# Optimization experiments

Measured on AMD Instinct MI355X. Metric: run time of the kernel, lower is better.

## Reference

```python
import jax, jax.numpy as jnp
import numpy as np

NEG = -9.0e15
EPS = 1e-5  # torch BatchNorm1d default eps


def _chain_idx(n):
    # chain graph with self loops; row-major nonzero ordering (matches torch .nonzero())
    rows, cols = [], []
    for i in range(n):
        for j in (i - 1, i, i + 1):
            if 0 <= j < n:
                rows.append(i); cols.append(j)
    return np.asarray(rows, np.int32), np.asarray(cols, np.int32)


def semgconv(x, W, e, rows, cols, n, b):
    # x: [B,N,Fin]; W: [2,Fin,Fout]; e: [nnz]; returns [B,N,Fout]
    h0 = jnp.einsum('bnf,fo->bno', x, W[0])
    h1 = jnp.einsum('bnf,fo->bno', x, W[1])
    logits = jnp.full((n, n), NEG, x.dtype).at[rows, cols].set(e)
    A = jax.nn.softmax(logits, axis=1)              # row-wise softmax over masked adjacency
    d = jnp.diagonal(A)                             # adj * I contribution
    A_off = A - jnp.diag(d)                         # adj * (1 - I)
    out = d[None, :, None] * h0 + jnp.einsum('ij,bjf->bif', A_off, h1)
    return out + b


def gblock(x, W, e, rows, cols, n, b, g, be):
    # SemGraphConv -> BatchNorm1d (training-mode batch stats over (B,N)) -> ReLU
    h = semgconv(x, W, e, rows, cols, n, b)
    mu = h.mean(axis=(0, 1))
    var = h.var(axis=(0, 1))
    h = g * (h - mu) * jax.lax.rsqrt(var + EPS) + be
    return jax.nn.relu(h)


def setup_inputs() -> dict:
    key = jax.random.key(0)
    ks = iter(jax.random.split(key, 40))
    B, NC, NS, H, HS = 4096, 32, 10, 160, 512  # HS = int(160/10*32)
    rc, cc = _chain_idx(NC)
    rs, cs = _chain_idx(NS)
    nnz_c, nnz_s = len(rc), len(rs)

    def w(shape, scale=0.1):
        return jax.random.normal(next(ks), shape, jnp.float32) * scale

    return dict(
        x_c=jax.random.normal(next(ks), (B, NC, 2), jnp.float32),
        x_s=jax.random.normal(next(ks), (B, NS, 2), jnp.float32),
        W_in=w((2, 2, H)), e_in=w((nnz_c,)) + 1.0, b_in=w((H,)),
        g_in=jnp.ones((H,), jnp.float32), be_in=jnp.zeros((H,), jnp.float32),
        W_s1=w((2, 2, HS)), e_s1=w((nnz_s,)) + 1.0, b_s1=w((HS,)),
        g_s1=jnp.ones((HS,), jnp.float32), be_s1=jnp.zeros((HS,), jnp.float32),
        W_c320=w((3, 2, 2 * H, H)), e_c320=w((3, nnz_c)) + 1.0, b_c320=w((3, H)),
        g_c320=jnp.ones((3, H), jnp.float32), be_c320=jnp.zeros((3, H), jnp.float32),
        W_c160=w((6, 2, H, H)), e_c160=w((6, nnz_c)) + 1.0, b_c160=w((6, H)),
        g_c160=jnp.ones((6, H), jnp.float32), be_c160=jnp.zeros((6, H), jnp.float32),
        W_s512=w((2, 2, HS, HS)), e_s512=w((2, nnz_s)) + 1.0, b_s512=w((2, HS)),
        g_s512=jnp.ones((2, HS), jnp.float32), be_s512=jnp.zeros((2, HS), jnp.float32),
        W_out=w((2, H, 2)), e_out=w((nnz_c,)) + 1.0, b_out=w((2,)),
        mc_r=jnp.asarray(rc), mc_c=jnp.asarray(cc),
        ms_r=jnp.asarray(rs), ms_c=jnp.asarray(cs),
    )


def reference(x_c, x_s, W_in, e_in, b_in, g_in, be_in,
              W_s1, e_s1, b_s1, g_s1, be_s1,
              W_c320, e_c320, b_c320, g_c320, be_c320,
              W_c160, e_c160, b_c160, g_c160, be_c160,
              W_s512, e_s512, b_s512, g_s512, be_s512,
              W_out, e_out, b_out, mc_r, mc_c, ms_r, ms_c):
    B, NC, NS, H = x_c.shape[0], 32, 10, 160
    c = gblock(x_c, W_in, e_in, mc_r, mc_c, NC, b_in, g_in, be_in)
    s = gblock(x_s, W_s1, e_s1, ms_r, ms_c, NS, b_s1, g_s1, be_s1)   # [B,10,512]
    for i in range(3):  # c_block1..3 interleaved with s_block2..3
        s_r = jnp.transpose(s, (0, 2, 1)).reshape(B, NC, H)          # [B,512,10] -> [B,32,160]
        c = gblock(jnp.concatenate([c, s_r], axis=2),
                   W_c320[i], e_c320[i], mc_r, mc_c, NC,
                   b_c320[i], g_c320[i], be_c320[i])
        h = gblock(c, W_c160[2 * i], e_c160[2 * i], mc_r, mc_c, NC,
                   b_c160[2 * i], g_c160[2 * i], be_c160[2 * i])
        h = gblock(h, W_c160[2 * i + 1], e_c160[2 * i + 1], mc_r, mc_c, NC,
                   b_c160[2 * i + 1], g_c160[2 * i + 1], be_c160[2 * i + 1])
        c = c + h                                                     # _ResGraphConv residual
        if i < 2:
            s = gblock(s, W_s512[i], e_s512[i], ms_r, ms_c, NS,
                       b_s512[i], g_s512[i], be_s512[i])
    return jax.nn.sigmoid(semgconv(c, W_out, e_out, mc_r, mc_c, NC, b_out))
```

## Files before the change

### kernel.cpp

```cpp
#include <hip/hip_runtime.h>
#include <hip/hip_bf16.h>

typedef __hip_bfloat16 bf16;
typedef unsigned short u16;
typedef __attribute__((ext_vector_type(8))) short short8;
typedef __attribute__((ext_vector_type(8))) unsigned short u16x8;
typedef __attribute__((ext_vector_type(4))) float f32x4;

#define B_SZ  4096
#define NCN   32
#define NSN   10
#define MC    (B_SZ*NCN)
#define MS    (B_SZ*NSN)
#define BUF_ELEMS 20971520UL

#define MODE_IN  0
#define MODE_PL  1
#define MODE_CC  2

#define DT_BF16  0
#define DT_F32   1
#define DT_PROBE 2

#define PART_SLOTS 163840
#define W_TOTAL    3411968

__device__ __forceinline__ float bf2f(bf16 v) { return __bfloat162float(v); }
__device__ __forceinline__ float ldv(const void* p, int dt, int idx) {
    return dt ? ((const float*)p)[idx] : bf2f(((const bf16*)p)[idx]);
}
__device__ __forceinline__ int resolve(int dt, const u16* probe) {
    return (dt == DT_PROBE) ? ((probe[0] == 0x3F80u) ? DT_BF16 : DT_F32) : dt;
}
__device__ __forceinline__ u16 f2bfbits(float f) {
    unsigned u = __builtin_bit_cast(unsigned, f);
    u += 0x7FFFu + ((u >> 16) & 1u);
    return (u16)(u >> 16);
}
__device__ __forceinline__ float bits2f(u16 u) {
    return __builtin_bit_cast(float, (unsigned)u << 16);
}
__device__ __forceinline__ size_t cfrag_addr(int r, int k) {
    int RT = r >> 8, within = r & 255;
    int g = ((within >> 6) << 2) | ((within >> 4) & 3);
    int tg = k >> 5, q = (k >> 3) & 3, j = k & 7;
    return ((((size_t)RT * 5 + tg) * 16 + g) * 64 + q * 16 + (r & 15)) * 8 + j;
}

struct WD { const void* src; int srcOff; int dstOff; int K; int F; };
struct WArgs { WD d[13]; };

__global__ void presplit_kernel(WArgs a, const u16* __restrict__ probe,
                                u16* __restrict__ Wf) {
    WD D = a.d[blockIdx.y];
    int nsteps = (D.K + 31) / 32;
    int total = (D.F / 32) * nsteps * 4096;
    int idx = blockIdx.x * blockDim.x + threadIdx.x;
    if (idx >= total) return;
    int dt = resolve(DT_PROBE, probe);
    int per = nsteps * 4096;
    int chunk = idx / per;  int rem = idx - chunk * per;
    int s = rem >> 12;      int slot = rem & 4095;
    int half = slot >> 11;  int sl = slot & 2047;
    int nt = sl >> 9;       int within = sl & 511;
    int lane = within >> 3; int j = within & 7;
    int q = lane >> 4, l15 = lane & 15;
    int plane = nt >> 1;
    int fcol = chunk * 32 + (nt & 1) * 16 + l15;
    int k = s * 32 + q * 8 + j;
    float v = (k < D.K) ? ldv(D.src, dt, D.srcOff + plane * D.K * D.F + k * D.F + fcol) : 0.f;
    u16 hb = f2bfbits(v);
    Wf[D.dstOff + idx] = half ? f2bfbits(v - bits2f(hb)) : hb;
}

struct CD { const void* e; int off; int n; };
struct CArgs { CD d[14]; };

__global__ void coeffs_all(CArgs a, const u16* __restrict__ probe, float* __restrict__ cfb) {
    CD D = a.d[blockIdx.x];
    float* cf = cfb + blockIdx.x * 96;
    int dt = resolve(DT_PROBE, probe);
    int i = threadIdx.x;
    if (i >= D.n) return;
    bool hasL = (i > 0), hasR = (i < D.n - 1);
    int off = D.off + ((i == 0) ? 0 : (3 * i - 1));
    float el = hasL ? ldv(D.e, dt, off) : 0.f;
    float es = ldv(D.e, dt, off + (hasL ? 1 : 0));
    float er = hasR ? ldv(D.e, dt, off + (hasL ? 2 : 1)) : 0.f;
    float m = es;
    if (hasL) m = fmaxf(m, el);
    if (hasR) m = fmaxf(m, er);
    float xl = hasL ? expf(el - m) : 0.f;
    float xs = expf(es - m);
    float xr = hasR ? expf(er - m) : 0.f;
    float inv = 1.f / (xl + xs + xr);
    cf[i]           = xl * inv;
    cf[D.n + i]     = xs * inv;
    cf[2 * D.n + i] = xr * inv;
}

template<int WAVES, int NODES, int KT, int TMODE, int AFRAG>
__global__ __launch_bounds__(WAVES * 64, (WAVES == 4) ? 4 : 3) void gemm_mfma(
    const u16* __restrict__ Wf, int wtOff,
    const u16* __restrict__ aHi, const u16* __restrict__ bHi2,
    const void* __restrict__ raw,
    const void* __restrict__ bias, int bOff,
    const u16* __restrict__ probe, const float* __restrict__ cf,
    u16* __restrict__ Thi,
    float* __restrict__ sumP, float* __restrict__ sqP, int F)
{
    constexpr int ROWS   = WAVES * 64;
    constexpr int nsteps = (KT + 31) / 32;
    constexpr int CHUNK  = (nsteps % 5 == 0) ? 5 : ((nsteps % 4 == 0) ? 4 : 1);
    constexpr int NCHUNK = nsteps / CHUNK;
    constexpr int NGRP   = WAVES * 4;
    constexpr int W_BYTES   = CHUNK * 8192;
    constexpr int VL_BYTES  = ROWS * 36 * 4;
    constexpr int RED_ONE   = 32 * (WAVES * 4) * 4;
    constexpr int EPI_BYTES = VL_BYTES + 2 * RED_ONE;
    constexpr int SMEM_SZ   = (W_BYTES > EPI_BYTES) ? W_BYTES : EPI_BYTES;

    const int tid  = threadIdx.x;
    const int wave = tid >> 6, lane = tid & 63;
    const int l15  = lane & 15, q = lane >> 4;

    const int NY   = F >> 5;
    const int nwg  = gridDim.x;
    const int NX   = nwg / NY;
    const int orig = blockIdx.x;
    const int xcd  = orig & 7, pos = orig >> 3;
    const int qch  = nwg >> 3, rch = nwg & 7;
    const int lin  = (xcd < rch ? xcd * (qch + 1)
                                : rch * (qch + 1) + (xcd - rch) * qch) + pos;
    const int bx   = lin / NY;
    const int by   = lin - bx * NY;
    const int f0   = by * 32;
    const int row0 = bx * ROWS;
    const int wdt  = resolve(DT_PROBE, probe);

    __shared__ __align__(16) char smem[SMEM_SZ];
    u16* Wt = (u16*)smem;
    float (*Vl)[36] = (float(*)[36])smem;
    float (*redS)[WAVES * 4] = (float(*)[WAVES * 4])(smem + VL_BYTES);
    float (*redQ)[WAVES * 4] = (float(*)[WAVES * 4])(smem + VL_BYTES + RED_ONE);

    const u16* wbase = Wf + wtOff + (size_t)by * nsteps * 4096;

    f32x4 acc[4][4];
#pragma unroll
    for (int a = 0; a < 4; ++a)
#pragma unroll
        for (int b = 0; b < 4; ++b) acc[a][b] = (f32x4){0.f, 0.f, 0.f, 0.f};

    if constexpr (TMODE == MODE_IN) {
        if (tid < 256) {
#pragma unroll
            for (int i = 0; i < 2; ++i) {
                int vs = i * 256 + tid;
                *(short8*)&Wt[vs * 8] = *(const short8*)(wbase + vs * 8);
            }
        }
        __syncthreads();
        short8 ahh[4], alo[4];
        const int kbase = q * 8;
#pragma unroll
        for (int mt = 0; mt < 4; ++mt) {
            int R = row0 + wave * 64 + mt * 16 + l15;
#pragma unroll
            for (int j = 0; j < 8; ++j) {
                int k = kbase + j;
                float v = (k < KT) ? ldv(raw, wdt, R * KT + k) : 0.f;
                u16 hb = f2bfbits(v);
                ahh[mt][j] = (short)hb;
                alo[mt][j] = (short)f2bfbits(v - bits2f(hb));
            }
        }
#pragma unroll
        for (int nt = 0; nt < 4; ++nt) {
            short8 bh = *(const short8*)&Wt[(nt * 64 + lane) * 8];
            short8 bl = *(const short8*)&Wt[2048 + (nt * 64 + lane) * 8];
#pragma unroll
            for (int mt = 0; mt < 4; ++mt) {
                acc[mt][nt] = __builtin_amdgcn_mfma_f32_16x16x32_bf16(ahh[mt], bh, acc[mt][nt], 0, 0, 0);
                acc[mt][nt] = __builtin_amdgcn_mfma_f32_16x16x32_bf16(ahh[mt], bl, acc[mt][nt], 0, 0, 0);
            }
#pragma unroll
            for (int mt = 0; mt < 4; ++mt)
                acc[mt][nt] = __builtin_amdgcn_mfma_f32_16x16x32_bf16(alo[mt], bh, acc[mt][nt], 0, 0, 0);
        }
        __syncthreads();
    } else {
        for (int c0 = 0; c0 < NCHUNK; ++c0) {
            if (tid < 256) {
                const u16* wc = wbase + c0 * CHUNK * 4096;
#pragma unroll
                for (int i = 0; i < CHUNK * 2; ++i) {
                    int vs = i * 256 + tid;
                    *(short8*)&Wt[vs * 8] = *(const short8*)(wc + vs * 8);
                }
            }
            __syncthreads();
#pragma unroll
            for (int sc = 0; sc < CHUNK; ++sc) {
                const int tg = c0 * CHUNK + sc;
                short8 ah[4];
                if constexpr (AFRAG == 1) {
#pragma unroll
                    for (int mt = 0; mt < 4; ++mt)
                        ah[mt] = *(const short8*)(aHi +
                            ((((size_t)bx * nsteps + tg) * NGRP) + (wave * 4 + mt)) * 512 + lane * 8);
                } else if constexpr (AFRAG == 3) {
                    const u16* base = (tg >= 5) ? bHi2 : aHi;
                    const int tgp = (tg >= 5) ? tg - 5 : tg;
#pragma unroll
                    for (int mt = 0; mt < 4; ++mt)
                        ah[mt] = *(const short8*)(base +
                            ((((size_t)bx * 5 + tgp) * 16) + (wave * 4 + mt)) * 512 + lane * 8);
                } else if constexpr (AFRAG == 2) {
                    if (tg >= 5) {
#pragma unroll
                        for (int mt = 0; mt < 4; ++mt)
                            ah[mt] = *(const short8*)(bHi2 +
                                ((((size_t)bx * 5 + (tg - 5)) * 16) + (wave * 4 + mt)) * 512 + lane * 8);
                    } else {
                        const int kbase = tg * 32 + q * 8;
#pragma unroll
                        for (int mt = 0; mt < 4; ++mt) {
                            size_t R = (size_t)(row0 + wave * 64 + mt * 16 + l15);
                            ah[mt] = *(const short8*)(aHi + R * 160 + kbase);
                        }
                    }
                } else {
                    const int kbase = tg * 32 + q * 8;
                    const u16* hp; int stride, col;
                    if (TMODE == MODE_CC && kbase >= 160) { hp = bHi2; stride = 160; col = kbase - 160; }
                    else { hp = aHi; stride = (TMODE == MODE_CC) ? 160 : KT; col = kbase; }
#pragma unroll
                    for (int mt = 0; mt < 4; ++mt) {
                        size_t R = (size_t)(row0 + wave * 64 + mt * 16 + l15);
                        ah[mt] = *(const short8*)(hp + R * stride + col);
                    }
                }
#pragma unroll
                for (int nt = 0; nt < 4; ++nt) {
                    short8 bh = *(const short8*)&Wt[sc * 4096 + (nt * 64 + lane) * 8];
                    short8 bl = *(const short8*)&Wt[sc * 4096 + 2048 + (nt * 64 + lane) * 8];
#pragma unroll
                    for (int mt = 0; mt < 4; ++mt) {
                        acc[mt][nt] = __builtin_amdgcn_mfma_f32_16x16x32_bf16(ah[mt], bh, acc[mt][nt], 0, 0, 0);
                        acc[mt][nt] = __builtin_amdgcn_mfma_f32_16x16x32_bf16(ah[mt], bl, acc[mt][nt], 0, 0, 0);
                    }
                }
            }
            __syncthreads();
        }
    }

#pragma unroll
    for (int mt = 0; mt < 4; ++mt)
#pragma unroll
        for (int vt = 0; vt < 2; ++vt)
#pragma unroll
            for (int j = 0; j < 4; ++j)
                Vl[wave * 64 + mt * 16 + q * 4 + j][vt * 16 + l15] = acc[mt][2 + vt][j];
    __syncthreads();
    float bv0 = ldv(bias, wdt, bOff + f0 + l15);
    float bv1 = ldv(bias, wdt, bOff + f0 + 16 + l15);
    float cS[2] = {0.f, 0.f}, cQ[2] = {0.f, 0.f};
#pragma unroll
    for (int mt = 0; mt < 4; ++mt) {
#pragma unroll
        for (int j = 0; j < 4; ++j) {
            int r = wave * 64 + mt * 16 + q * 4 + j;
            int i = r % NODES;
            int rm = (i > 0)         ? r - 1 : r;
            int rp = (i < NODES - 1) ? r + 1 : r;
            float cl = cf[i], cs = cf[NODES + i], cr = cf[2 * NODES + i];
#pragma unroll
            for (int nt = 0; nt < 2; ++nt) {
                int c = nt * 16 + l15;
                float h = cs * acc[mt][nt][j] + cl * Vl[rm][c] + cr * Vl[rp][c]
                        + (nt ? bv1 : bv0);
                Thi[(size_t)(row0 + r) * F + f0 + c] = f2bfbits(h);
                cS[nt] += h; cQ[nt] += h * h;
            }
        }
    }
    redS[l15][wave * 4 + q] = cS[0];      redQ[l15][wave * 4 + q] = cQ[0];
    redS[16 + l15][wave * 4 + q] = cS[1]; redQ[16 + l15][wave * 4 + q] = cQ[1];
    __syncthreads();
    if (tid < 32) {
        float s = 0.f, t2 = 0.f;
#pragma unroll
        for (int t = 0; t < WAVES * 4; ++t) { s += redS[tid][t]; t2 += redQ[tid][t]; }
        sumP[(f0 + tid) * NX + bx] = s;
        sqP [(f0 + tid) * NX + bx] = t2;
    }
}

__global__ void bn_finalize(const float* __restrict__ sumP, const float* __restrict__ sqP,
                            int gridX, const void* __restrict__ g, int gOff,
                            const void* __restrict__ be, int beOff,
                            const u16* __restrict__ probe, float invM,
                            float* __restrict__ scale, float* __restrict__ shift) {
    int f = blockIdx.x;
    int t = threadIdx.x;
    __shared__ float ss[256], qq[256];
    float s = 0.f, q = 0.f;
    for (int i = t; i < gridX; i += 256) { s += sumP[f * gridX + i]; q += sqP[f * gridX + i]; }
    ss[t] = s; qq[t] = q;
    __syncthreads();
    for (int o = 128; o > 0; o >>= 1) {
        if (t < o) { ss[t] += ss[t + o]; qq[t] += qq[t + o]; }
        __syncthreads();
    }
    if (t == 0) {
        int dt = resolve(DT_PROBE, probe);
        float mu  = ss[0] * invM;
        float var = fmaf(-mu, mu, qq[0] * invM);
        float inv = rsqrtf(var + 1e-5f);
        float sc  = ldv(g, dt, gOff + f) * inv;
        scale[f] = sc;
        shift[f] = ldv(be, dt, beOff + f) - mu * sc;
    }
}

__global__ void bn_apply_frag(const u16* __restrict__ Thi,
                              const float* __restrict__ scale, const float* __restrict__ shift,
                              const u16* __restrict__ resHi,
                              u16* __restrict__ dst, int total8) {
    int slot = blockIdx.x * blockDim.x + threadIdx.x;
    if (slot >= total8) return;
    int lane = slot & 63; int rest = slot >> 6;
    int g = rest & 15;    int rs = rest >> 4;
    int s = rs % 5;       int RT = rs / 5;
    int l15 = lane & 15, q = lane >> 4;
    int row = RT * 256 + (g >> 2) * 64 + (g & 3) * 16 + l15;
    int col = s * 32 + q * 8;
    u16x8 th = *(const u16x8*)(Thi + (size_t)row * 160 + col);
    float v[8];
#pragma unroll
    for (int j = 0; j < 8; ++j)
        v[j] = fmaxf(fmaf(scale[col + j], bits2f(th[j]), shift[col + j]), 0.f);
    if (resHi) {
        u16x8 rh = *(const u16x8*)(resHi + (size_t)slot * 8);
#pragma unroll
        for (int j = 0; j < 8; ++j) v[j] += bits2f(rh[j]);
    }
    u16x8 oh;
#pragma unroll
    for (int j = 0; j < 8; ++j) oh[j] = f2bfbits(v[j]);
    *(u16x8*)(dst + (size_t)slot * 8) = oh;
}

__global__ __launch_bounds__(256) void bn_apply_s(
    const u16* __restrict__ Thi,
    const float* __restrict__ scale, const float* __restrict__ shift,
    u16* __restrict__ dstS, u16* __restrict__ dstR) {
    __shared__ u16 tile[10 * 520];
    const int t = threadIdx.x;
    const int b = blockIdx.x;
    const size_t baseT = (size_t)b * 5120;
#pragma unroll
    for (int i = 0; i < 3; ++i) {
        int slot = t + 256 * i;
        if (slot < 640) {
            int s0 = slot * 8;
            int qn = s0 >> 9, p0 = s0 & 511;
            u16x8 th = *(const u16x8*)(Thi + baseT + s0);
            u16x8 oh;
#pragma unroll
            for (int j = 0; j < 8; ++j)
                oh[j] = f2bfbits(fmaxf(fmaf(scale[p0 + j], bits2f(th[j]), shift[p0 + j]), 0.f));
            *(u16x8*)&tile[qn * 520 + p0] = oh;
            int within = (b & 31) * 10 + qn;
            int g = (within >> 6) * 4 + ((within >> 4) & 3);
            int l15 = within & 15;
            int tg = p0 >> 5, q = (p0 >> 3) & 3;
            size_t slotF = ((((size_t)(b >> 5) * 16 + tg) * 20) + g) * 64 + q * 16 + l15;
            *(u16x8*)(dstS + slotF * 8) = oh;
        }
    }
    __syncthreads();
#pragma unroll
    for (int i = 0; i < 3; ++i) {
        int slot = t + 256 * i;
        if (slot < 640) {
            int o0 = slot * 8;
            int rw = o0 / 160, cl0 = o0 - rw * 160;
            u16x8 oh;
#pragma unroll
            for (int j = 0; j < 8; ++j) {
                int o = o0 + j;
                int p = o / 10, qn = o - p * 10;
                oh[j] = tile[qn * 520 + p];
            }
            int within = (b & 7) * 32 + rw;
            int g = (within >> 6) * 4 + ((within >> 4) & 3);
            int l15 = within & 15;
            int tg = cl0 >> 5, q = (cl0 >> 3) & 3;
            size_t slotF = ((((size_t)(b >> 3) * 5 + tg) * 16) + g) * 64 + q * 16 + l15;
            *(u16x8*)(dstR + slotF * 8) = oh;
        }
    }
}

__global__ void out_kernel(const u16* __restrict__ cHi,
                           const void* __restrict__ W, const void* __restrict__ bias,
                           const float* __restrict__ cf,
                           const u16* __restrict__ probe,
                           void* __restrict__ out) {
    int gtid = blockIdx.x * blockDim.x + threadIdx.x;
    int r = gtid >> 6;
    int lane = gtid & 63;
    if (r >= MC) return;
    int wDt = resolve(DT_PROBE, probe);
    int i = r & 31;
    float cl = cf[i], cs = cf[32 + i], cr = cf[64 + i];
    int rm = (i > 0)  ? r - 1 : r;
    int rp = (i < 31) ? r + 1 : r;
    float ps0 = 0.f, ps1 = 0.f, pn0 = 0.f, pn1 = 0.f;
    for (int k = lane; k < 160; k += 64) {
        float xs = bits2f(cHi[cfrag_addr(r, k)]);
        float xn = cl * bits2f(cHi[cfrag_addr(rm, k)])
                 + cr * bits2f(cHi[cfrag_addr(rp, k)]);
        float w00 = ldv(W, wDt, k * 2),       w01 = ldv(W, wDt, k * 2 + 1);
        float w10 = ldv(W, wDt, 320 + k * 2), w11 = ldv(W, wDt, 320 + k * 2 + 1);
        ps0 = fmaf(xs, w00, ps0);
        ps1 = fmaf(xs, w01, ps1);
        pn0 = fmaf(xn, w10, pn0);
        pn1 = fmaf(xn, w11, pn1);
    }
#pragma unroll
    for (int off = 32; off > 0; off >>= 1) {
        ps0 += __shfl_down(ps0, off, 64);
        ps1 += __shfl_down(ps1, off, 64);
        pn0 += __shfl_down(pn0, off, 64);
        pn1 += __shfl_down(pn1, off, 64);
    }
    if (lane == 0) {
        float v0 = cs * ps0 + pn0 + ldv(bias, wDt, 0);
        float v1 = cs * ps1 + pn1 + ldv(bias, wDt, 1);
        float s0 = 1.f / (1.f + expf(-v0));
        float s1 = 1.f / (1.f + expf(-v1));
        if (probe[0] == 0x3F80u) {
            ((bf16*)out)[r * 2 + 0] = __float2bfloat16(s0);
            ((bf16*)out)[r * 2 + 1] = __float2bfloat16(s1);
        } else {
            ((float*)out)[r * 2 + 0] = s0;
            ((float*)out)[r * 2 + 1] = s1;
        }
    }
}

extern "C" void kernel_launch(void* const* d_in, const int* in_sizes, int n_in,
                              void* d_out, int out_size, void* d_ws, size_t ws_size,
                              hipStream_t stream) {
    const u16* probe = (const u16*)d_in[5];

    float* sumP  = (float*)d_ws;
    float* sqP   = sumP + PART_SLOTS;
    float* scale = sqP + PART_SLOTS;
    float* shift = scale + 512;
    float* cfb   = shift + 512;
    u16*   Wf    = (u16*)(cfb + 14 * 96);
    char*  p     = (char*)(Wf + W_TOTAL);

    size_t PL = 2 * BUF_ELEMS;
    u16 *Thi = (u16*)p; p += PL;
    u16 *Chi = (u16*)p; p += PL;
    u16 *Shi = (u16*)p; p += PL;
    u16 *Hhi = (u16*)p; p += PL;
    (void)ws_size;

    WArgs wa;
    int wo = 0; int di = 0;
    auto addW = [&](const void* src, int sOff, int K, int F) {
        wa.d[di++] = WD{src, sOff, wo, K, F};
        wo += (F / 32) * ((K + 31) / 32) * 4096;
    };
    addW(d_in[2], 0, 2, 160);
    addW(d_in[7], 0, 2, 512);
    for (int i = 0; i < 3; ++i) addW(d_in[12], i * 102400, 320, 160);
    for (int i = 0; i < 6; ++i) addW(d_in[17], i * 51200, 160, 160);
    for (int i = 0; i < 2; ++i) addW(d_in[22], i * 524288, 512, 512);
    presplit_kernel<<<dim3(4096, 13), 256, 0, stream>>>(wa, probe, Wf);

    CArgs ca;
    int ci = 0;
    auto addC = [&](const void* e, int off, int n) { ca.d[ci++] = CD{e, off, n}; };
    addC(d_in[3], 0, 32);
    addC(d_in[8], 0, 10);
    for (int i = 0; i < 3; ++i) addC(d_in[13], i * 94, 32);
    for (int i = 0; i < 6; ++i) addC(d_in[18], i * 94, 32);
    for (int i = 0; i < 2; ++i) addC(d_in[23], i * 28, 10);
    addC(d_in[28], 0, 32);
    coeffs_all<<<14, 64, 0, stream>>>(ca, probe, cfb);

    const int wtIn = 0, wtS1 = 20480, wtC320 = 86016, wtC160 = 700416, wtS512 = 1314816;

    auto post_c = [&](const void* g, int gOff, const void* be, int beOff,
                      u16* dHi, const u16* rHi) {
        bn_finalize<<<160, 256, 0, stream>>>(sumP, sqP, 512, g, gOff, be, beOff,
                                             probe, 1.f / (float)MC, scale, shift);
        bn_apply_frag<<<MC * 160 / 8 / 256, 256, 0, stream>>>(
            Thi, scale, shift, rHi, dHi, MC * 160 / 8);
    };
    auto post_s = [&](const void* g, int gOff, const void* be, int beOff) {
        bn_finalize<<<512, 256, 0, stream>>>(sumP, sqP, 128, g, gOff, be, beOff,
                                             probe, 1.f / (float)MS, scale, shift);
        bn_apply_s<<<B_SZ, 256, 0, stream>>>(Thi, scale, shift, Shi, Hhi);
    };

    const dim3 gc(512 * 5), gs(128 * 16);

    gemm_mfma<4, 32, 2, MODE_IN, 0><<<gc, 256, 0, stream>>>(
        Wf, wtIn, nullptr, nullptr, d_in[0], d_in[4], 0, probe, cfb + 0 * 96,
        Thi, sumP, sqP, 160);
    post_c(d_in[5], 0, d_in[6], 0, Chi, nullptr);

    gemm_mfma<5, 10, 2, MODE_IN, 0><<<gs, 320, 0, stream>>>(
        Wf, wtS1, nullptr, nullptr, d_in[1], d_in[9], 0, probe, cfb + 1 * 96,
        Thi, sumP, sqP, 512);
    post_s(d_in[10], 0, d_in[11], 0);

    for (int i = 0; i < 3; ++i) {
        gemm_mfma<4, 32, 320, MODE_CC, 3><<<gc, 256, 0, stream>>>(
            Wf, wtC320 + i * 204800, Chi, Hhi, nullptr, d_in[14], i * 160,
            probe, cfb + (2 + i) * 96, Thi, sumP, sqP, 160);
        post_c(d_in[15], i * 160, d_in[16], i * 160, Chi, nullptr);

        gemm_mfma<4, 32, 160, MODE_PL, 1><<<gc, 256, 0, stream>>>(
            Wf, wtC160 + (2 * i) * 102400, Chi, nullptr, nullptr, d_in[19], (2 * i) * 160,
            probe, cfb + (5 + 2 * i) * 96, Thi, sumP, sqP, 160);
        post_c(d_in[20], (2 * i) * 160, d_in[21], (2 * i) * 160, Hhi, nullptr);

        gemm_mfma<4, 32, 160, MODE_PL, 1><<<gc, 256, 0, stream>>>(
            Wf, wtC160 + (2 * i + 1) * 102400, Hhi, nullptr, nullptr, d_in[19], (2 * i + 1) * 160,
            probe, cfb + (6 + 2 * i) * 96, Thi, sumP, sqP, 160);
        post_c(d_in[20], (2 * i + 1) * 160, d_in[21], (2 * i + 1) * 160, Chi, Chi);

        if (i < 2) {
            gemm_mfma<5, 10, 512, MODE_PL, 1><<<gs, 320, 0, stream>>>(
                Wf, wtS512 + i * 1048576, Shi, nullptr, nullptr, d_in[24], i * 512,
                probe, cfb + (11 + i) * 96, Thi, sumP, sqP, 512);
            post_s(d_in[25], i * 512, d_in[26], i * 512);
        }
    }

    out_kernel<<<(MC * 64 + 255) / 256, 256, 0, stream>>>(Chi, d_in[27], d_in[29],
                                                          cfb + 13 * 96, probe, d_out);
}
```

Baseline: 1.108 ms.

## Store pre-BN activations directly in MFMA fragment layout

The GEMM epilogue now writes the pre-normalization tensor in the fragment-tiled layout used by the next GEMM's A operand, instead of row-major. The BN apply kernels then read it contiguously by slot, with no row/column remapping. The unused AFRAG==2 path is removed. The goal is coalesced, streaming loads in the apply kernels; the cost is scattered 2-byte stores in the epilogue, and the leftover unused index computations in bn_apply_frag look fragile.

```diff
diff --git a/kernel.cpp b/kernel.cpp
--- a/kernel.cpp
+++ b/kernel.cpp
@@ -216,20 +216,6 @@
                     for (int mt = 0; mt < 4; ++mt)
                         ah[mt] = *(const short8*)(base +
                             ((((size_t)bx * 5 + tgp) * 16) + (wave * 4 + mt)) * 512 + lane * 8);
-                } else if constexpr (AFRAG == 2) {
-                    if (tg >= 5) {
-#pragma unroll
-                        for (int mt = 0; mt < 4; ++mt)
-                            ah[mt] = *(const short8*)(bHi2 +
-                                ((((size_t)bx * 5 + (tg - 5)) * 16) + (wave * 4 + mt)) * 512 + lane * 8);
-                    } else {
-                        const int kbase = tg * 32 + q * 8;
-#pragma unroll
-                        for (int mt = 0; mt < 4; ++mt) {
-                            size_t R = (size_t)(row0 + wave * 64 + mt * 16 + l15);
-                            ah[mt] = *(const short8*)(aHi + R * 160 + kbase);
-                        }
-                    }
                 } else {
                     const int kbase = tg * 32 + q * 8;
                     const u16* hp; int stride, col;
@@ -264,6 +250,9 @@
             for (int j = 0; j < 4; ++j)
                 Vl[wave * 64 + mt * 16 + q * 4 + j][vt * 16 + l15] = acc[mt][2 + vt][j];
     __syncthreads();
+    const size_t rbase = (WAVES == 4)
+        ? (((size_t)bx * 5 + by) * 16) * 512
+        : (((size_t)bx * 16 + by) * 20) * 512;
     float bv0 = ldv(bias, wdt, bOff + f0 + l15);
     float bv1 = ldv(bias, wdt, bOff + f0 + 16 + l15);
     float cS[2] = {0.f, 0.f}, cQ[2] = {0.f, 0.f};
@@ -281,7 +270,9 @@
                 int c = nt * 16 + l15;
                 float h = cs * acc[mt][nt][j] + cl * Vl[rm][c] + cr * Vl[rp][c]
                         + (nt ? bv1 : bv0);
-                Thi[(size_t)(row0 + r) * F + f0 + c] = f2bfbits(h);
+                int qp = nt * 2 + (l15 >> 3), jp = l15 & 7;
+                Thi[rbase + (((size_t)(wave * 4 + mt) * 64) + qp * 16 + (q * 4 + j)) * 8 + jp]
+                    = f2bfbits(h);
                 cS[nt] += h; cQ[nt] += h * h;
             }
         }
@@ -331,13 +322,13 @@
                               u16* __restrict__ dst, int total8) {
     int slot = blockIdx.x * blockDim.x + threadIdx.x;
     if (slot >= total8) return;
-    int lane = slot & 63; int rest = slot >> 6;
-    int g = rest & 15;    int rs = rest >> 4;
-    int s = rs % 5;       int RT = rs / 5;
-    int l15 = lane & 15, q = lane >> 4;
-    int row = RT * 256 + (g >> 2) * 64 + (g & 3) * 16 + l15;
-    int col = s * 32 + q * 8;
-    u16x8 th = *(const u16x8*)(Thi + (size_t)row * 160 + col);
+    int lane = slot & 63; int rest = slot >> 4;
+    int s = (slot >> 10) % 5;
+    int tg = ((slot >> 6) >> 4) % 5;
+    int q = lane >> 4;
+    int col = tg * 32 + q * 8;
+    (void)rest; (void)s;
+    u16x8 th = *(const u16x8*)(Thi + (size_t)slot * 8);
     float v[8];
 #pragma unroll
     for (int j = 0; j < 8; ++j)
@@ -360,24 +351,23 @@
     __shared__ u16 tile[10 * 520];
     const int t = threadIdx.x;
     const int b = blockIdx.x;
-    const size_t baseT = (size_t)b * 5120;
 #pragma unroll
     for (int i = 0; i < 3; ++i) {
         int slot = t + 256 * i;
         if (slot < 640) {
             int s0 = slot * 8;
             int qn = s0 >> 9, p0 = s0 & 511;
-            u16x8 th = *(const u16x8*)(Thi + baseT + s0);
-            u16x8 oh;
-#pragma unroll
-            for (int j = 0; j < 8; ++j)
-                oh[j] = f2bfbits(fmaxf(fmaf(scale[p0 + j], bits2f(th[j]), shift[p0 + j]), 0.f));
-            *(u16x8*)&tile[qn * 520 + p0] = oh;
             int within = (b & 31) * 10 + qn;
             int g = (within >> 6) * 4 + ((within >> 4) & 3);
             int l15 = within & 15;
             int tg = p0 >> 5, q = (p0 >> 3) & 3;
             size_t slotF = ((((size_t)(b >> 5) * 16 + tg) * 20) + g) * 64 + q * 16 + l15;
+            u16x8 th = *(const u16x8*)(Thi + slotF * 8);
+            u16x8 oh;
+#pragma unroll
+            for (int j = 0; j < 8; ++j)
+                oh[j] = f2bfbits(fmaxf(fmaf(scale[p0 + j], bits2f(th[j]), shift[p0 + j]), 0.f));
+            *(u16x8*)&tile[qn * 520 + p0] = oh;
             *(u16x8*)(dstS + slotF * 8) = oh;
         }
     }
```

Result: no change. 1.110 ms (+0.1%).
